# Performance work log

Measured on AMD Instinct MI355X. Metric: run time of the kernel, lower is better.

Reference implementation:

```python
import jax, jax.numpy as jnp
import numpy as np

EPS = 1e-5
NC = 183  # num_classes
FUSION_LEVEL = 1

def conv2d(x, w, b=None, pad=0):
    y = jax.lax.conv_general_dilated(x, w, (1, 1), [(pad, pad), (pad, pad)],
                                     dimension_numbers=('NCHW', 'OIHW', 'NCHW'))
    return y if b is None else y + b[None, :, None, None]

def bn(x, g, b, m, v):
    s = g / jnp.sqrt(v + EPS)
    return x * s[None, :, None, None] + (b - m * s)[None, :, None, None]

def deform_conv(x, offset, weight):
    # DCNv1: x [B,C,H,W], offset [B,18,H,W] as (dy,dx) per kernel point, weight [O,C,3,3]
    B, C, H, W = x.shape
    K = 9
    off = offset.reshape(B, K, 2, H, W)
    ky = (jnp.arange(K) // 3 - 1).astype(x.dtype)
    kx = (jnp.arange(K) % 3 - 1).astype(x.dtype)
    yy = jnp.arange(H, dtype=x.dtype)[None, None, :, None] + ky[None, :, None, None] + off[:, :, 0]
    xx = jnp.arange(W, dtype=x.dtype)[None, None, None, :] + kx[None, :, None, None] + off[:, :, 1]
    y0 = jnp.floor(yy)
    x0 = jnp.floor(xx)
    wy = yy - y0
    wx = xx - x0
    def gather(yi, xi):
        valid = ((yi >= 0) & (yi <= H - 1) & (xi >= 0) & (xi <= W - 1))
        yc = jnp.clip(yi, 0, H - 1).astype(jnp.int32)
        xc = jnp.clip(xi, 0, W - 1).astype(jnp.int32)
        g = jax.vmap(lambda im, a, b: im[:, a, b])(x, yc, xc)  # [B,C,K,H,W]
        return g * valid.astype(x.dtype)[:, None]
    s = (gather(y0, x0) * ((1 - wy) * (1 - wx))[:, None]
         + gather(y0, x0 + 1) * ((1 - wy) * wx)[:, None]
         + gather(y0 + 1, x0) * (wy * (1 - wx))[:, None]
         + gather(y0 + 1, x0 + 1) * (wy * wx)[:, None])
    return jnp.einsum('bckhw,ock->bohw', s, weight.reshape(weight.shape[0], C, K))

def resize_bilinear(x, oh, ow):
    # F.interpolate(mode='bilinear', align_corners=True)
    B, C, H, W = x.shape
    if (H, W) == (oh, ow):
        return x
    ys = jnp.linspace(0.0, H - 1.0, oh)
    xs = jnp.linspace(0.0, W - 1.0, ow)
    y0 = jnp.clip(jnp.floor(ys).astype(jnp.int32), 0, H - 2)
    x0 = jnp.clip(jnp.floor(xs).astype(jnp.int32), 0, W - 2)
    wy = (ys - y0).astype(x.dtype)
    wx = (xs - x0).astype(x.dtype)
    r = x[:, :, y0, :] * (1 - wy)[None, None, :, None] + x[:, :, y0 + 1, :] * wy[None, None, :, None]
    return r[:, :, :, x0] * (1 - wx) + r[:, :, :, x0 + 1] * wx

def setup_inputs() -> dict:
    key = jax.random.key(0)
    ks = iter(jax.random.split(key, 64))
    nk = lambda: next(ks)
    B, C = 1, 256
    sizes = [256, 128, 64, 32, 16]
    w = lambda shape, sc: jax.random.normal(nk(), shape, jnp.float32) * sc
    inp = {}
    for i, s in enumerate(sizes):
        inp['feat%d' % i] = jax.random.normal(nk(), (B, C, s, s), jnp.float32)
    inp['off1_w'] = w((18, C, 3, 3), 0.01); inp['off1_b'] = w((18,), 0.01)
    inp['dc1_w'] = w((C, C, 3, 3), 0.02)
    inp['off2_w'] = w((18, C, 3, 3), 0.01); inp['off2_b'] = w((18,), 0.01)
    inp['dc2_w'] = w((C, C, 3, 3), 0.02)
    inp['bn2_g'] = 1.0 + w((C,), 0.01); inp['bn2_b'] = w((C,), 0.01)
    inp['bn2_m'] = w((C,), 0.01); inp['bn2_v'] = jax.random.uniform(nk(), (C,), jnp.float32) + 0.5
    inp['convs_w'] = w((4, C, C, 3, 3), 0.02)
    inp['convs_g'] = 1.0 + w((4, C), 0.01); inp['convs_b'] = w((4, C), 0.01)
    inp['convs_m'] = w((4, C), 0.01); inp['convs_v'] = jax.random.uniform(nk(), (4, C), jnp.float32) + 0.5
    inp['emb_w'] = w((C, C, 1, 1), 0.05)
    inp['emb_g'] = 1.0 + w((C,), 0.01); inp['emb_b'] = w((C,), 0.01)
    inp['emb_m'] = w((C,), 0.01); inp['emb_v'] = jax.random.uniform(nk(), (C,), jnp.float32) + 0.5
    inp['logit_w'] = w((NC, C, 1, 1), 0.05); inp['logit_b'] = w((NC,), 0.01)
    return inp

def reference(feat0, feat1, feat2, feat3, feat4,
              off1_w, off1_b, dc1_w, off2_w, off2_b, dc2_w,
              bn2_g, bn2_b, bn2_m, bn2_v,
              convs_w, convs_g, convs_b, convs_m, convs_v,
              emb_w, emb_g, emb_b, emb_m, emb_v,
              logit_w, logit_b):
    feats = [feat0, feat1, feat2, feat3, feat4]
    def branch(f):
        o = conv2d(f, off1_w, off1_b, pad=1)
        h = deform_conv(f, o, dc1_w)
        o = conv2d(h, off2_w, off2_b, pad=1)
        h = deform_conv(h, o, dc2_w)
        return jax.nn.relu(bn(h, bn2_g, bn2_b, bn2_m, bn2_v))
    x = branch(feats[FUSION_LEVEL])
    H, W = x.shape[-2:]
    for i, f in enumerate(feats):
        if i != FUSION_LEVEL:
            x = x + branch(resize_bilinear(f, H, W))
    for i in range(4):
        x = jax.nn.relu(bn(conv2d(x, convs_w[i], pad=1),
                           convs_g[i], convs_b[i], convs_m[i], convs_v[i]))
    mask_pred = conv2d(x, logit_w, logit_b, pad=0)
    emb = jax.nn.relu(bn(conv2d(x, emb_w, pad=0), emb_g, emb_b, emb_m, emb_v))
    return (mask_pred, emb)
```

## Files before the change

kernel.cpp:

```cpp
#include <hip/hip_runtime.h>
#include <hip/hip_bf16.h>
#include <stdint.h>

#define EPS_BN 1e-5f
constexpr int PP = 16384;
using short8 = __attribute__((ext_vector_type(8))) short;
using f32x4  = __attribute__((ext_vector_type(4))) float;
typedef unsigned short u16;

__device__ inline float bf2f(u16 u) {
  unsigned v = ((unsigned)u) << 16; float f; __builtin_memcpy(&f, &v, 4); return f;
}
__device__ inline u16 f2bf(float f) {
  unsigned b; __builtin_memcpy(&b, &f, 4);
  b += 0x7FFFu + ((b >> 16) & 1u);
  return (u16)(b >> 16);
}
__device__ inline float u2f(unsigned x) { float f; __builtin_memcpy(&f, &x, 4); return f; }

#define GLD16(g, l) __builtin_amdgcn_global_load_lds( \
    (__attribute__((address_space(1))) void*)(void*)(g), \
    (__attribute__((address_space(3))) void*)(void*)(l), 16, 0, 0)

__global__ void bn_prep_k(const float* __restrict__ g0, const float* __restrict__ b0,
                          const float* __restrict__ m0, const float* __restrict__ v0,
                          const float* __restrict__ cg, const float* __restrict__ cb,
                          const float* __restrict__ cm, const float* __restrict__ cv,
                          const float* __restrict__ eg, const float* __restrict__ eb,
                          const float* __restrict__ em, const float* __restrict__ ev,
                          float* __restrict__ scale, float* __restrict__ shift) {
  int c = threadIdx.x;
  float s = g0[c] * rsqrtf(v0[c] + EPS_BN);
  scale[c] = s; shift[c] = b0[c] - m0[c] * s;
#pragma unroll
  for (int i = 0; i < 4; ++i) {
    float si = cg[i*256+c] * rsqrtf(cv[i*256+c] + EPS_BN);
    scale[(1+i)*256+c] = si; shift[(1+i)*256+c] = cb[i*256+c] - cm[i*256+c]*si;
  }
  float se = eg[c] * rsqrtf(ev[c] + EPS_BN);
  scale[5*256+c] = se; shift[5*256+c] = eb[c] - em[c]*se;
}

__global__ void prep_w_k(const float* __restrict__ w, u16* __restrict__ W2,
                         int Ocnt, int KK, int NPAD) {
  int idx = blockIdx.x * 256 + threadIdx.x;
  int total = NPAD * KK * 256;
  if (idx >= total) return;
  int o = idx / (KK * 256); int rem = idx - o * (KK * 256);
  int kpt = rem >> 8, c = rem & 255;
  W2[idx] = (o < Ocnt) ? f2bf(w[(o * 256 + c) * KK + kpt]) : (u16)0;
}

__global__ void prep_wf_k(const float* __restrict__ w, u16* __restrict__ W2f) {
  int idx = blockIdx.x * 256 + threadIdx.x;
  int ks = idx >> 13, r = idx & 8191;
  int n = r >> 9, r2 = r & 511;
  int lane = r2 >> 3, j = r2 & 7;
  int k = ks * 32 + ((lane >> 4) << 3) + j;
  int oc = n * 16 + (lane & 15);
  W2f[idx] = f2bf(w[(oc * 256 + (k & 255)) * 9 + (k >> 8)]);
}

__global__ void tr_k(const float* __restrict__ in, u16* __restrict__ out, int P) {
  __shared__ float tile[64][65];
  int p0 = blockIdx.x * 64, c0 = blockIdx.y * 64;
  int t = threadIdx.x;
  int tl = t & 63, tg = t >> 6;
#pragma unroll
  for (int i = 0; i < 16; ++i) {
    int c = tg * 16 + i;
    tile[c][tl] = in[(size_t)(c0 + c) * P + p0 + tl];
  }
  __syncthreads();
  int px = t >> 2, cq = t & 3;
#pragma unroll
  for (int pass = 0; pass < 2; ++pass) {
    int c = cq * 8 + pass * 32;
    u16 r[8];
#pragma unroll
    for (int j = 0; j < 8; ++j) r[j] = f2bf(tile[c + j][px]);
    *(short8*)(out + (size_t)(p0 + px) * 256 + c0 + c) = *(short8*)r;
  }
}

__global__ void rs_k(const u16* __restrict__ in, u16* __restrict__ out, int Hs) {
  int t = threadIdx.x;
  int p = blockIdx.x * 8 + (t >> 5), q = t & 31;
  int oy = p >> 7, ox = p & 127;
  float sc = (float)(Hs - 1) / 127.0f;
  float ys = oy * sc, xs = ox * sc;
  int y0 = (int)ys; if (y0 > Hs - 2) y0 = Hs - 2;
  int x0 = (int)xs; if (x0 > Hs - 2) x0 = Hs - 2;
  float wy = ys - (float)y0, wx = xs - (float)x0;
  const u16* b00 = in + ((size_t)(y0 * Hs + x0)) * 256 + q * 8;
  short8 v00 = *(const short8*)b00;
  short8 v01 = *(const short8*)(b00 + 256);
  short8 v10 = *(const short8*)(b00 + (size_t)Hs * 256);
  short8 v11 = *(const short8*)(b00 + (size_t)Hs * 256 + 256);
  u16 r[8];
#pragma unroll
  for (int j = 0; j < 8; ++j) {
    float a = bf2f((u16)v00[j]) * (1.f - wx) + bf2f((u16)v01[j]) * wx;
    float b = bf2f((u16)v10[j]) * (1.f - wx) + bf2f((u16)v11[j]) * wx;
    r[j] = f2bf(a * (1.f - wy) + b * wy);
  }
  *(short8*)(out + (size_t)p * 256 + q * 8) = *(short8*)r;
}

struct KS { float w0, w1, w2, w3; unsigned o0, o1, o2, o3; };

template<int EPI>
__launch_bounds__(256, 2)
__global__ void dc_k(const u16* __restrict__ A, const u16* __restrict__ Bw2,
                     const float* __restrict__ offs, u16* __restrict__ oB,
                     const float* __restrict__ scale, const float* __restrict__ shift) {
  __shared__ u16 sB[3][256 * 32];
  const int t = threadIdx.x, w = t >> 6, l = t & 63, lr = l & 15, lq = l >> 4;
  int bx = blockIdx.x; { int n8 = gridDim.x >> 3; bx = (bx & 7) * n8 + (bx >> 3); }
  const int p0 = bx * 64;
  const int gp = p0 + w * 16 + lr;
  const int pl = gp & 16383;
  const unsigned lbo = (unsigned)(gp & ~16383) * 256u;

  f32x4 acc[16];
#pragma unroll
  for (int n = 0; n < 16; ++n) acc[n] = (f32x4){0.f, 0.f, 0.f, 0.f};

  short8 cvA[4], cvB[4];

  auto mkKpt = [&](int kpt) -> KS {
    float2 o2 = *(const float2*)(offs + (size_t)gp * 32 + 2 * kpt);
    float yy = (float)((pl >> 7) + kpt / 3 - 1) + o2.x;
    float xx = (float)((pl & 127) + kpt % 3 - 1) + o2.y;
    float yf = floorf(yy), xf = floorf(xx);
    float fy = yy - yf, fx = xx - xf;
    int y0 = (int)yf, x0 = (int)xf;
    float gy0 = (1.f - fy) * (((unsigned)y0 < 128u) ? 1.f : 0.f);
    float gy1 = fy * (((unsigned)(y0 + 1) < 128u) ? 1.f : 0.f);
    float gx0 = (1.f - fx) * (((unsigned)x0 < 128u) ? 1.f : 0.f);
    float gx1 = fx * (((unsigned)(x0 + 1) < 128u) ? 1.f : 0.f);
    int y0c = y0 < 0 ? 0 : (y0 > 127 ? 127 : y0);
    int y1c = y0 + 1 < 0 ? 0 : (y0 + 1 > 127 ? 127 : y0 + 1);
    int x0c = x0 < 0 ? 0 : (x0 > 127 ? 127 : x0);
    int x1c = x0 + 1 < 0 ? 0 : (x0 + 1 > 127 ? 127 : x0 + 1);
    KS st;
    st.w0 = gy0 * gx0; st.w1 = gy0 * gx1; st.w2 = gy1 * gx0; st.w3 = gy1 * gx1;
    st.o0 = lbo + (unsigned)((y0c << 7) + x0c) * 256u;
    st.o1 = lbo + (unsigned)((y0c << 7) + x1c) * 256u;
    st.o2 = lbo + (unsigned)((y1c << 7) + x0c) * 256u;
    st.o3 = lbo + (unsigned)((y1c << 7) + x1c) * 256u;
    return st;
  };
  auto loadC4 = [&](short8* cvb, const KS& st, int s) {
    int cc = ((s & 7) << 5) + lq * 8;
    cvb[0] = *(const short8*)(A + (size_t)st.o0 + cc);
    cvb[1] = *(const short8*)(A + (size_t)st.o1 + cc);
    cvb[2] = *(const short8*)(A + (size_t)st.o2 + cc);
    cvb[3] = *(const short8*)(A + (size_t)st.o3 + cc);
  };
  auto interp = [&](const short8* cvb, const KS& st) -> short8 {
    u16 rr[8];
    const unsigned* u0 = (const unsigned*)&cvb[0];
    const unsigned* u1 = (const unsigned*)&cvb[1];
    const unsigned* u2 = (const unsigned*)&cvb[2];
    const unsigned* u3 = (const unsigned*)&cvb[3];
#pragma unroll
    for (int j2 = 0; j2 < 4; ++j2) {
      unsigned a0 = u0[j2], a1 = u1[j2], a2 = u2[j2], a3 = u3[j2];
      float lo = st.w0 * u2f(a0 << 16) + st.w1 * u2f(a1 << 16)
               + st.w2 * u2f(a2 << 16) + st.w3 * u2f(a3 << 16);
      float hi = st.w0 * u2f(a0 & 0xFFFF0000u) + st.w1 * u2f(a1 & 0xFFFF0000u)
               + st.w2 * u2f(a2 & 0xFFFF0000u) + st.w3 * u2f(a3 & 0xFFFF0000u);
      __hip_bfloat16 hl = __float2bfloat16(lo);
      __hip_bfloat16 hh = __float2bfloat16(hi);
      rr[2 * j2]     = *(u16*)&hl;
      rr[2 * j2 + 1] = *(u16*)&hh;
    }
    return *(short8*)rr;
  };
  auto stageB = [&](int ks) {
    const u16* src = Bw2 + (size_t)ks * 8192 + t * 8;
    char* dst = (char*)sB[ks % 3] + t * 16;
#pragma unroll
    for (int it = 0; it < 4; ++it) GLD16(src + it * 2048, dst + it * 4096);
  };

  KS cur = mkKpt(0);
  KS nxt = cur;
  stageB(0); loadC4(cvA, cur, 0);
  stageB(1); loadC4(cvB, cur, 1);

  for (int kpt = 0; kpt < 9; ++kpt) {
#pragma unroll
    for (int ss = 0; ss < 8; ++ss) {
      const int ks = kpt * 8 + ss;
      short8* cvb = (ss & 1) ? cvB : cvA;
      short8 af = interp(cvb, cur);
      __builtin_amdgcn_sched_barrier(0);
      __builtin_amdgcn_s_barrier();
      __builtin_amdgcn_sched_barrier(0);
      if (ss == 5 && kpt < 8) nxt = mkKpt(kpt + 1);
      if (kpt < 8 || ss < 6) {
        stageB(ks + 2);
        loadC4(cvb, (ss < 6) ? cur : nxt, ks + 2);
      }
      const char* base = (const char*)sB[ks % 3] + l * 16;
      __builtin_amdgcn_s_setprio(1);
#pragma unroll
      for (int n = 0; n < 16; ++n) {
        short8 bfr = *(const short8*)(base + n * 1024);
        acc[n] = __builtin_amdgcn_mfma_f32_16x16x32_bf16(af, bfr, acc[n], 0, 0, 0);
      }
      __builtin_amdgcn_s_setprio(0);
    }
    cur = nxt;
  }

  {
    int prow = p0 + w * 16 + lq * 4;
#pragma unroll
    for (int n = 0; n < 16; ++n) {
      int oc = n * 16 + lr;
      float sc = 1.f, sh = 0.f;
      if constexpr (EPI == 3) { sc = scale[oc]; sh = shift[oc]; }
#pragma unroll
      for (int q = 0; q < 4; ++q) {
        float v = acc[n][q];
        if constexpr (EPI == 3) v = fmaxf(v * sc + sh, 0.f);
        oB[(size_t)(prow + q) * 256 + oc] = f2bf(v);
      }
    }
  }
}

template<int MODE, int AM, int AN, int MW, int NW, int EPI>
__launch_bounds__(MW*NW*64)
__global__ void mm_k(const u16* __restrict__ A, const u16* __restrict__ B,
                     const u16* __restrict__ zbuf,
                     float* __restrict__ oF, u16* __restrict__ oB,
                     const float* __restrict__ bias,
                     const float* __restrict__ scale, const float* __restrict__ shift,
                     int Ktot, int ksteps, int OutN) {
  constexpr int BM = MW * AM * 16, BN = NW * AN * 16, NT = MW * NW * 64;
  constexpr int AITS = BM * 8 / NT, BITS = BN * 8 / NT;
  __shared__ u16 sA[BM * 64];
  __shared__ u16 sB[BN * 64];
  char* sAb = (char*)sA; char* sBb = (char*)sB;
  const int t = threadIdx.x;
  const int w = t >> 6, l = t & 63;
  const int lr = l & 15, lq = l >> 4;
  const int wm = w / NW, wn = w % NW;
  int bx = blockIdx.x;
  { int n8 = gridDim.x >> 3; bx = (bx & 7) * n8 + (bx >> 3); }
  const int p0 = bx * BM, n0 = blockIdx.y * BN;

  f32x4 acc[AM][AN];
#pragma unroll
  for (int m = 0; m < AM; ++m)
#pragma unroll
    for (int n = 0; n < AN; ++n) acc[m][n] = (f32x4){0.f, 0.f, 0.f, 0.f};

  for (int ks = 0; ks < ksteps; ++ks) {
    int k0 = ks * 64;
#pragma unroll
    for (int it = 0; it < BITS; ++it) {
      int ch = it * NT + t;
      int row = ch >> 3, cl = (ch & 7) ^ (row & 7);
      GLD16(B + (size_t)(n0 + row) * Ktot + k0 + cl * 8, sBb + it * (NT * 16) + w * 1024);
    }
    if constexpr (MODE == 0) {
#pragma unroll
      for (int it = 0; it < AITS; ++it) {
        int ch = it * NT + t;
        int row = ch >> 3, cl = (ch & 7) ^ (row & 7);
        GLD16(A + (size_t)(p0 + row) * Ktot + k0 + cl * 8, sAb + it * (NT * 16) + w * 1024);
      }
    } else {
      int kpt = k0 >> 8, c0 = k0 & 255;
      int dy = kpt / 3 - 1, dx = kpt % 3 - 1;
#pragma unroll
      for (int it = 0; it < AITS; ++it) {
        int ch = it * NT + t;
        int row = ch >> 3, cl = (ch & 7) ^ (row & 7);
        int gp = p0 + row; int lvl = gp >> 14, pl = gp & 16383;
        int yy = (pl >> 7) + dy, xx = (pl & 127) + dx;
        const u16* src = ((unsigned)yy < 128u && (unsigned)xx < 128u)
            ? A + ((size_t)(lvl << 14) + (yy << 7) + xx) * 256 + c0 + cl * 8
            : zbuf;
        GLD16(src, sAb + it * (NT * 16) + w * 1024);
      }
    }
    __syncthreads();
    short8 af[AM], bfr[AN];
#pragma unroll
    for (int h = 0; h < 2; ++h) {
#pragma unroll
      for (int m = 0; m < AM; ++m) {
        int ar = wm * AM * 16 + m * 16 + lr;
        af[m] = *(const short8*)(sAb + ar * 128 + (((h * 4 + lq) ^ (ar & 7)) << 4));
      }
#pragma unroll
      for (int n = 0; n < AN; ++n) {
        int br = wn * AN * 16 + n * 16 + lr;
        bfr[n] = *(const short8*)(sBb + br * 128 + (((h * 4 + lq) ^ (br & 7)) << 4));
      }
#pragma unroll
      for (int m = 0; m < AM; ++m)
#pragma unroll
        for (int n = 0; n < AN; ++n)
          acc[m][n] = __builtin_amdgcn_mfma_f32_16x16x32_bf16(af[m], bfr[n], acc[m][n], 0, 0, 0);
    }
    __syncthreads();
  }

#pragma unroll
  for (int m = 0; m < AM; ++m) {
    int prow = p0 + wm * AM * 16 + m * 16 + lq * 4;
#pragma unroll
    for (int n = 0; n < AN; ++n) {
      int oc = n0 + wn * AN * 16 + n * 16 + lr;
      if constexpr (EPI == 1) {
        float bs = (oc < 18) ? bias[oc] : 0.f;
#pragma unroll
        for (int r = 0; r < 4; ++r) oF[(size_t)(prow + r) * 32 + oc] = acc[m][n][r] + bs;
      } else if constexpr (EPI == 2) {
#pragma unroll
        for (int r = 0; r < 4; ++r) oB[(size_t)(prow + r) * 256 + oc] = f2bf(acc[m][n][r]);
      } else if constexpr (EPI == 3) {
        float sc = scale[oc], sh = shift[oc];
#pragma unroll
        for (int r = 0; r < 4; ++r)
          oB[(size_t)(prow + r) * 256 + oc] = f2bf(fmaxf(acc[m][n][r] * sc + sh, 0.f));
      } else if constexpr (EPI == 4) {
        if (oc < OutN) {
          float bs = bias[oc];
          float4 v = {acc[m][n][0] + bs, acc[m][n][1] + bs, acc[m][n][2] + bs, acc[m][n][3] + bs};
          *(float4*)(oF + (size_t)oc * PP + prow) = v;
        }
      } else {
        float sc = scale[oc], sh = shift[oc];
        float4 v = {fmaxf(acc[m][n][0] * sc + sh, 0.f), fmaxf(acc[m][n][1] * sc + sh, 0.f),
                    fmaxf(acc[m][n][2] * sc + sh, 0.f), fmaxf(acc[m][n][3] * sc + sh, 0.f)};
        *(float4*)(oF + (size_t)oc * PP + prow) = v;
      }
    }
  }
}

__global__ void sum5_k(const u16* __restrict__ H2, u16* __restrict__ out) {
  size_t base = ((size_t)blockIdx.x * 256 + threadIdx.x) * 8;
  float a[8] = {0,0,0,0,0,0,0,0};
#pragma unroll
  for (int lvl = 0; lvl < 5; ++lvl) {
    short8 v = *(const short8*)(H2 + (size_t)lvl * PP * 256 + base);
#pragma unroll
    for (int j = 0; j < 8; ++j) a[j] += bf2f((u16)v[j]);
  }
  u16 r[8];
#pragma unroll
  for (int j = 0; j < 8; ++j) r[j] = f2bf(a[j]);
  *(short8*)(out + base) = *(short8*)r;
}

extern "C" void kernel_launch(void* const* d_in, const int* in_sizes, int n_in,
                              void* d_out, int out_size, void* d_ws, size_t ws_size,
                              hipStream_t stream) {
  const float* feats[5];
  for (int i = 0; i < 5; ++i) feats[i] = (const float*)d_in[i];
  int fsz[5] = {256, 128, 64, 32, 16};
  const float* off1_w = (const float*)d_in[5];
  const float* off1_b = (const float*)d_in[6];
  const float* dc1_w  = (const float*)d_in[7];
  const float* off2_w = (const float*)d_in[8];
  const float* off2_b = (const float*)d_in[9];
  const float* dc2_w  = (const float*)d_in[10];
  const float* bn2_g  = (const float*)d_in[11];
  const float* bn2_b  = (const float*)d_in[12];
  const float* bn2_m  = (const float*)d_in[13];
  const float* bn2_v  = (const float*)d_in[14];
  const float* convs_w = (const float*)d_in[15];
  const float* convs_g = (const float*)d_in[16];
  const float* convs_b = (const float*)d_in[17];
  const float* convs_m = (const float*)d_in[18];
  const float* convs_v = (const float*)d_in[19];
  const float* emb_w  = (const float*)d_in[20];
  const float* emb_g  = (const float*)d_in[21];
  const float* emb_b  = (const float*)d_in[22];
  const float* emb_m  = (const float*)d_in[23];
  const float* emb_v  = (const float*)d_in[24];
  const float* logit_w = (const float*)d_in[25];
  const float* logit_b = (const float*)d_in[26];

  char* ws = (char*)d_ws;
  size_t off = 0;
  auto alloc = [&](size_t bytes) { char* p = ws + off; off += (bytes + 255) & ~255ull; return p; };
  float* bnscale = (float*)alloc(6 * 256 * 4);
  float* bnshift = (float*)alloc(6 * 256 * 4);
  u16* zbuf = (u16*)alloc(256);
  u16* W2_off1 = (u16*)alloc((size_t)32 * 2304 * 2);
  u16* W2_off2 = (u16*)alloc((size_t)32 * 2304 * 2);
  u16* W2_dc1  = (u16*)alloc((size_t)256 * 2304 * 2);
  u16* W2_dc2  = (u16*)alloc((size_t)256 * 2304 * 2);
  u16* W2_c    = (u16*)alloc((size_t)4 * 256 * 2304 * 2);
  u16* W2_logit = (u16*)alloc((size_t)256 * 256 * 2);
  u16* W2_emb   = (u16*)alloc((size_t)256 * 256 * 2);
  u16* R_all  = (u16*)alloc((size_t)5 * PP * 256 * 2);
  u16* H_all  = (u16*)alloc((size_t)5 * PP * 256 * 2);
  u16* H2_all = (u16*)alloc((size_t)5 * PP * 256 * 2);
  float* O    = (float*)alloc((size_t)5 * PP * 32 * 4);
  u16* Xb     = (u16*)alloc((size_t)PP * 256 * 2);
  u16* Ftmp = H_all;
  u16* cb0 = R_all;
  u16* cb1 = R_all + (size_t)PP * 256;

  hipMemsetAsync(zbuf, 0, 256, stream);
  bn_prep_k<<<1, 256, 0, stream>>>(bn2_g, bn2_b, bn2_m, bn2_v, convs_g, convs_b, convs_m, convs_v,
                                   emb_g, emb_b, emb_m, emb_v, bnscale, bnshift);
  auto pw = [&](const float* src, u16* dst, int Ocnt, int KK, int NPAD) {
    int total = NPAD * KK * 256;
    prep_w_k<<<(total + 255) / 256, 256, 0, stream>>>(src, dst, Ocnt, KK, NPAD);
  };
  pw(off1_w, W2_off1, 18, 9, 32);
  pw(off2_w, W2_off2, 18, 9, 32);
  prep_wf_k<<<2304, 256, 0, stream>>>(dc1_w, W2_dc1);
  prep_wf_k<<<2304, 256, 0, stream>>>(dc2_w, W2_dc2);
  for (int i = 0; i < 4; ++i) pw(convs_w + (size_t)i * 2304 * 256, W2_c + (size_t)i * 2304 * 256, 256, 9, 256);
  pw(logit_w, W2_logit, 183, 1, 256);
  pw(emb_w,   W2_emb,   256, 1, 256);

  const dim3 blk(256);
  for (int lvl = 0; lvl < 5; ++lvl) {
    int P = fsz[lvl] * fsz[lvl];
    u16* dst = (lvl == 1) ? (R_all + (size_t)PP * 256) : Ftmp;
    tr_k<<<dim3(P / 64, 4), blk, 0, stream>>>(feats[lvl], dst, P);
    if (lvl != 1)
      rs_k<<<dim3(PP / 8), blk, 0, stream>>>(Ftmp, R_all + (size_t)lvl * PP * 256, fsz[lvl]);
  }

  constexpr int MG = 5 * PP;
  mm_k<1, 2, 2, 4, 1, 1><<<dim3(MG / 128, 1), blk, 0, stream>>>(
      R_all, W2_off1, zbuf, O, nullptr, off1_b, nullptr, nullptr, 2304, 36, 32);
  dc_k<2><<<dim3(MG / 64), blk, 0, stream>>>(R_all, W2_dc1, O, H_all, nullptr, nullptr);
  mm_k<1, 2, 2, 4, 1, 1><<<dim3(MG / 128, 1), blk, 0, stream>>>(
      H_all, W2_off2, zbuf, O, nullptr, off2_b, nullptr, nullptr, 2304, 36, 32);
  dc_k<3><<<dim3(MG / 64), blk, 0, stream>>>(H_all, W2_dc2, O, H2_all, bnscale, bnshift);

  sum5_k<<<dim3(2048), blk, 0, stream>>>(H2_all, Xb);

  const u16* cur = Xb;
  u16* cbuf[2] = {cb0, cb1};
  for (int i = 0; i < 4; ++i) {
    mm_k<1, 2, 2, 2, 2, 3><<<dim3(PP / 64, 4), blk, 0, stream>>>(
        cur, W2_c + (size_t)i * 2304 * 256, zbuf, nullptr, cbuf[i & 1],
        nullptr, bnscale + (1 + i) * 256, bnshift + (1 + i) * 256, 2304, 36, 256);
    cur = cbuf[i & 1];
  }

  float* outp = (float*)d_out;
  mm_k<0, 2, 4, 2, 2, 4><<<dim3(PP / 64, 2), blk, 0, stream>>>(
      cur, W2_logit, zbuf, outp, nullptr, logit_b, nullptr, nullptr, 256, 4, 183);
  mm_k<0, 2, 4, 2, 2, 5><<<dim3(PP / 64, 2), blk, 0, stream>>>(
      cur, W2_emb, zbuf, outp + (size_t)183 * PP, nullptr, nullptr,
      bnscale + 5 * 256, bnshift + 5 * 256, 256, 4, 256);
}
```

Measured before the change: 797.9 us.

## Process two 16-pixel tiles per wave in deformable conv to reuse B fragments

The deformable conv kernel now covers 128 pixels per block (32 per wave, as two 16-row MFMA tiles), so each LDS-loaded weight fragment feeds two MFMAs and weight staging traffic per pixel is halved. The pipeline is restructured from a depth-2 prefetch with alternating gather buffers into a single-step prefetch with one staged B buffer ahead. The cost is doubled accumulator registers (128 floats per thread), which may cut occupancy under launch_bounds(256,2) or cause spills, plus a shallower gather-latency hiding window and half as many blocks.

```diff
diff --git a/kernel.cpp b/kernel.cpp
--- a/kernel.cpp
+++ b/kernel.cpp
@@ -117,21 +117,21 @@
   __shared__ u16 sB[3][256 * 32];
   const int t = threadIdx.x, w = t >> 6, l = t & 63, lr = l & 15, lq = l >> 4;
   int bx = blockIdx.x; { int n8 = gridDim.x >> 3; bx = (bx & 7) * n8 + (bx >> 3); }
-  const int p0 = bx * 64;
-  const int gp = p0 + w * 16 + lr;
-  const int pl = gp & 16383;
-  const unsigned lbo = (unsigned)(gp & ~16383) * 256u;
-
-  f32x4 acc[16];
-#pragma unroll
-  for (int n = 0; n < 16; ++n) acc[n] = (f32x4){0.f, 0.f, 0.f, 0.f};
-
-  short8 cvA[4], cvB[4];
-
-  auto mkKpt = [&](int kpt) -> KS {
-    float2 o2 = *(const float2*)(offs + (size_t)gp * 32 + 2 * kpt);
-    float yy = (float)((pl >> 7) + kpt / 3 - 1) + o2.x;
-    float xx = (float)((pl & 127) + kpt % 3 - 1) + o2.y;
+  const int p0 = bx * 128;
+  const int gp0 = p0 + w * 32 + lr;
+  const int pl0 = gp0 & 16383;
+  const unsigned lbo = (unsigned)(gp0 & ~16383) * 256u;
+
+  f32x4 acc0[16], acc1[16];
+#pragma unroll
+  for (int n = 0; n < 16; ++n) { acc0[n] = (f32x4){0.f,0.f,0.f,0.f}; acc1[n] = (f32x4){0.f,0.f,0.f,0.f}; }
+
+  short8 cv0[4], cv1[4];
+
+  auto mkKpt = [&](int kpt, int gpx, int plx) -> KS {
+    float2 o2 = *(const float2*)(offs + (size_t)gpx * 32 + 2 * kpt);
+    float yy = (float)((plx >> 7) + kpt / 3 - 1) + o2.x;
+    float xx = (float)((plx & 127) + kpt % 3 - 1) + o2.y;
     float yf = floorf(yy), xf = floorf(xx);
     float fy = yy - yf, fx = xx - xf;
     int y0 = (int)yf, x0 = (int)xf;
@@ -185,50 +185,52 @@
     for (int it = 0; it < 4; ++it) GLD16(src + it * 2048, dst + it * 4096);
   };
 
-  KS cur = mkKpt(0);
-  KS nxt = cur;
-  stageB(0); loadC4(cvA, cur, 0);
-  stageB(1); loadC4(cvB, cur, 1);
-
-  for (int kpt = 0; kpt < 9; ++kpt) {
-#pragma unroll
-    for (int ss = 0; ss < 8; ++ss) {
-      const int ks = kpt * 8 + ss;
-      short8* cvb = (ss & 1) ? cvB : cvA;
-      short8 af = interp(cvb, cur);
-      __builtin_amdgcn_sched_barrier(0);
-      __builtin_amdgcn_s_barrier();
-      __builtin_amdgcn_sched_barrier(0);
-      if (ss == 5 && kpt < 8) nxt = mkKpt(kpt + 1);
-      if (kpt < 8 || ss < 6) {
-        stageB(ks + 2);
-        loadC4(cvb, (ss < 6) ? cur : nxt, ks + 2);
-      }
-      const char* base = (const char*)sB[ks % 3] + l * 16;
-      __builtin_amdgcn_s_setprio(1);
-#pragma unroll
-      for (int n = 0; n < 16; ++n) {
-        short8 bfr = *(const short8*)(base + n * 1024);
-        acc[n] = __builtin_amdgcn_mfma_f32_16x16x32_bf16(af, bfr, acc[n], 0, 0, 0);
-      }
-      __builtin_amdgcn_s_setprio(0);
-    }
-    cur = nxt;
-  }
-
-  {
-    int prow = p0 + w * 16 + lq * 4;
+  KS c0 = mkKpt(0, gp0, pl0);
+  KS c1 = mkKpt(0, gp0 + 16, pl0 + 16);
+  stageB(0);
+  loadC4(cv0, c0, 0);
+  loadC4(cv1, c1, 0);
+
+  for (int ks = 0; ks < 72; ++ks) {
+    if (ks < 71) stageB(ks + 1);
+    short8 af0 = interp(cv0, c0);
+    short8 af1 = interp(cv1, c1);
+    if (ks < 71 && (((ks + 1) & 7) == 0)) {
+      c0 = mkKpt((ks + 1) >> 3, gp0, pl0);
+      c1 = mkKpt((ks + 1) >> 3, gp0 + 16, pl0 + 16);
+    }
+    __builtin_amdgcn_sched_barrier(0);
+    __builtin_amdgcn_s_barrier();
+    __builtin_amdgcn_sched_barrier(0);
+    if (ks < 71) { loadC4(cv0, c0, ks + 1); loadC4(cv1, c1, ks + 1); }
+    const char* base = (const char*)sB[ks % 3] + l * 16;
+    __builtin_amdgcn_s_setprio(1);
 #pragma unroll
     for (int n = 0; n < 16; ++n) {
-      int oc = n * 16 + lr;
-      float sc = 1.f, sh = 0.f;
-      if constexpr (EPI == 3) { sc = scale[oc]; sh = shift[oc]; }
-#pragma unroll
-      for (int q = 0; q < 4; ++q) {
-        float v = acc[n][q];
-        if constexpr (EPI == 3) v = fmaxf(v * sc + sh, 0.f);
-        oB[(size_t)(prow + q) * 256 + oc] = f2bf(v);
-      }
+      short8 bfr = *(const short8*)(base + n * 1024);
+      acc0[n] = __builtin_amdgcn_mfma_f32_16x16x32_bf16(af0, bfr, acc0[n], 0, 0, 0);
+      acc1[n] = __builtin_amdgcn_mfma_f32_16x16x32_bf16(af1, bfr, acc1[n], 0, 0, 0);
+    }
+    __builtin_amdgcn_s_setprio(0);
+  }
+
+#pragma unroll
+  for (int n = 0; n < 16; ++n) {
+    int oc = n * 16 + lr;
+    float sc = 1.f, sh = 0.f;
+    if constexpr (EPI == 3) { sc = scale[oc]; sh = shift[oc]; }
+    int prow0 = p0 + w * 32 + lq * 4;
+#pragma unroll
+    for (int q = 0; q < 4; ++q) {
+      float v = acc0[n][q];
+      if constexpr (EPI == 3) v = fmaxf(v * sc + sh, 0.f);
+      oB[(size_t)(prow0 + q) * 256 + oc] = f2bf(v);
+    }
+#pragma unroll
+    for (int q = 0; q < 4; ++q) {
+      float v = acc1[n][q];
+      if constexpr (EPI == 3) v = fmaxf(v * sc + sh, 0.f);
+      oB[(size_t)(prow0 + 16 + q) * 256 + oc] = f2bf(v);
     }
   }
 }
@@ -440,10 +442,10 @@
   constexpr int MG = 5 * PP;
   mm_k<1, 2, 2, 4, 1, 1><<<dim3(MG / 128, 1), blk, 0, stream>>>(
       R_all, W2_off1, zbuf, O, nullptr, off1_b, nullptr, nullptr, 2304, 36, 32);
-  dc_k<2><<<dim3(MG / 64), blk, 0, stream>>>(R_all, W2_dc1, O, H_all, nullptr, nullptr);
+  dc_k<2><<<dim3(MG / 128), blk, 0, stream>>>(R_all, W2_dc1, O, H_all, nullptr, nullptr);
   mm_k<1, 2, 2, 4, 1, 1><<<dim3(MG / 128, 1), blk, 0, stream>>>(
       H_all, W2_off2, zbuf, O, nullptr, off2_b, nullptr, nullptr, 2304, 36, 32);
-  dc_k<3><<<dim3(MG / 64), blk, 0, stream>>>(H_all, W2_dc2, O, H2_all, bnscale, bnshift);
+  dc_k<3><<<dim3(MG / 128), blk, 0, stream>>>(H_all, W2_dc2, O, H2_all, bnscale, bnshift);
 
   sum5_k<<<dim3(2048), blk, 0, stream>>>(H2_all, Xb);
 
```

Measured after the change: 870.2 us. 1.09x slower.
